# Kernel tuning notes

Measured on AMD Instinct MI355X. Metric: run time of the kernel, lower is better.

The kernel has to match this reference:

```python
import jax, jax.numpy as jnp
import numpy as np

LODS = [16, 32, 64, 128, 256]
SCENE_SCALE = 4.0
DESC = 4
N = 2_000_000
# 8 corner offsets of a voxel, bit-decoded: (x, y, z) in {0,1}^3
_CORNERS = jnp.asarray([[(i >> 2) & 1, (i >> 1) & 1, i & 1] for i in range(8)], dtype=jnp.int32)  # (8,3)


def setup_inputs() -> dict:
    key = jax.random.key(0)
    ks = jax.random.split(key, 2 + len(LODS))
    inp = {
        "pts": jax.random.normal(ks[0], (N, 3), dtype=jnp.float32),
        "d": jax.random.normal(ks[1], (N, 3), dtype=jnp.float32),
    }
    # codebook init mirrors torch: zeros + 0.01 * randn, shape (LOD^3, desc)
    for i, res in enumerate(LODS):
        inp[f"codebook_{i}"] = jax.random.normal(ks[2 + i], (res ** 3, DESC), dtype=jnp.float32) * 0.01
    return inp


def _trilerp(res, codebook, pts01):
    """NGLOD-style dense-grid trilinear interpolation.
    pts01: (N,3) in [0,1]; codebook: (res^3, DESC). Returns (N, DESC)."""
    pos = pts01 * (res - 1)                                   # (N,3) in [0, res-1]
    c0 = jnp.clip(jnp.floor(pos).astype(jnp.int32), 0, res - 2)
    frac = pos - c0.astype(pos.dtype)                         # (N,3) in [0,1]
    idx = c0[:, None, :] + _CORNERS[None, :, :]               # (N,8,3)
    flat = (idx[..., 0] * res + idx[..., 1]) * res + idx[..., 2]  # (N,8) row-major x*res^2+y*res+z
    # trilinear weights: prod over axes of (frac if corner bit set else 1-frac)
    w = jnp.prod(jnp.where(_CORNERS[None] == 1, frac[:, None, :], 1.0 - frac[:, None, :]), axis=-1)  # (N,8)
    return jnp.einsum('nkd,nk->nd', codebook[flat], w)        # gather + weighted sum


def reference(pts, d, codebook_0, codebook_1, codebook_2, codebook_3, codebook_4):
    cbs = (codebook_0, codebook_1, codebook_2, codebook_3, codebook_4)
    p = pts / SCENE_SCALE
    mask = jnp.all(jnp.abs(p) < 0.5, axis=-1)                 # inside unit cube
    p01 = jnp.clip(p + 0.5, 0.0, 1.0)                         # clamp keeps OOB points index-safe; masked out below
    feats = _trilerp(LODS[0], cbs[0], p01)
    for res, cb in zip(LODS[1:], cbs[1:]):
        feats = feats + _trilerp(res, cb, p01)                # sum features across LODs
    color = jnp.where(mask[:, None], feats[:, 0:3], 0.0)      # masked scatter into zero buffer
    log_sigma = jnp.where(mask, feats[:, 3], -100000.0)       # exp(-1e5) underflows to 0, as in torch
    return color, jnp.exp(log_sigma)[:, None]
```

## Files before the change

kernel.cpp:

```cpp
#include <hip/hip_runtime.h>
#include <math.h>

static constexpr float kSceneScale = 4.0f;
static constexpr int   kG     = 16;
static constexpr int   kNBins = kG * kG * kG + 1;
static constexpr int   kNB    = 256;
static constexpr int   kDirectThresh = 48;

static constexpr int kS4 = 18;
static constexpr int kS3 = 10;
static constexpr int kS2 = 6;
static constexpr int kS1 = 4;
static constexpr int kS0 = 3;

__device__ __forceinline__ void fma4(float4& acc, float w, const float4& c) {
    acc.x = fmaf(w, c.x, acc.x);
    acc.y = fmaf(w, c.y, acc.y);
    acc.z = fmaf(w, c.z, acc.z);
    acc.w = fmaf(w, c.w, acc.w);
}

__device__ __forceinline__ unsigned bf16r(float f) {
    unsigned u = __float_as_uint(f);
    return (u + 0x7FFFu + ((u >> 16) & 1u)) >> 16;
}
__device__ __forceinline__ unsigned pk2(float lo, float hi) {
    return bf16r(lo) | (bf16r(hi) << 16);
}
__device__ __forceinline__ float4 bfdec(uint2 w) {
    float4 r;
    r.x = __uint_as_float(w.x << 16);
    r.y = __uint_as_float(w.x & 0xFFFF0000u);
    r.z = __uint_as_float(w.y << 16);
    r.w = __uint_as_float(w.y & 0xFFFF0000u);
    return r;
}

template <int RES>
__device__ __forceinline__ void trilerp_acc(const float4* __restrict__ cb,
                                            float x, float y, float z,
                                            float4& acc) {
    const float s = (float)(RES - 1);
    float fx = x * s, fy = y * s, fz = z * s;
    int x0 = min((int)fx, RES - 2);
    int y0 = min((int)fy, RES - 2);
    int z0 = min((int)fz, RES - 2);
    float tx = fx - (float)x0;
    float ty = fy - (float)y0;
    float tz = fz - (float)z0;
    int base = (x0 * RES + y0) * RES + z0;
    float4 c000 = cb[base];
    float4 c001 = cb[base + 1];
    float4 c010 = cb[base + RES];
    float4 c011 = cb[base + RES + 1];
    float4 c100 = cb[base + RES * RES];
    float4 c101 = cb[base + RES * RES + 1];
    float4 c110 = cb[base + RES * RES + RES];
    float4 c111 = cb[base + RES * RES + RES + 1];
    float wx0 = 1.0f - tx, wx1 = tx;
    float wy0 = 1.0f - ty, wy1 = ty;
    float wz0 = 1.0f - tz, wz1 = tz;
    fma4(acc, wx0 * wy0 * wz0, c000);
    fma4(acc, wx0 * wy0 * wz1, c001);
    fma4(acc, wx0 * wy1 * wz0, c010);
    fma4(acc, wx0 * wy1 * wz1, c011);
    fma4(acc, wx1 * wy0 * wz0, c100);
    fma4(acc, wx1 * wy0 * wz1, c101);
    fma4(acc, wx1 * wy1 * wz0, c110);
    fma4(acc, wx1 * wy1 * wz1, c111);
}

__device__ __forceinline__ void load_p01(const float* __restrict__ pts, int i,
                                         float& x, float& y, float& z, bool& inside) {
    float px = pts[3 * i + 0] * (1.0f / kSceneScale);
    float py = pts[3 * i + 1] * (1.0f / kSceneScale);
    float pz = pts[3 * i + 2] * (1.0f / kSceneScale);
    inside = (fabsf(px) < 0.5f) && (fabsf(py) < 0.5f) && (fabsf(pz) < 0.5f);
    x = fminf(fmaxf(px + 0.5f, 0.0f), 1.0f);
    y = fminf(fmaxf(py + 0.5f, 0.0f), 1.0f);
    z = fminf(fmaxf(pz + 0.5f, 0.0f), 1.0f);
}

__device__ __forceinline__ unsigned point_key(const float* __restrict__ pts, int i) {
    float x, y, z; bool inside;
    load_p01(pts, i, x, y, z, inside);
    if (!inside) return (unsigned)(kNBins - 1);
    int bx = min((int)(x * kG), kG - 1);
    int by = min((int)(y * kG), kG - 1);
    int bz = min((int)(z * kG), kG - 1);
    return (unsigned)((bx * kG + by) * kG + bz);
}

__global__ __launch_bounds__(256) void keys_hist_kernel(
        const float* __restrict__ pts, unsigned* __restrict__ keys,
        unsigned* __restrict__ blockHist, int n, int chunk) {
    __shared__ unsigned hist[kNBins];
    int tid = threadIdx.x;
    for (int j = tid; j < kNBins; j += 256) hist[j] = 0;
    __syncthreads();
    int beg = blockIdx.x * chunk;
    int end = min(n, beg + chunk);
    for (int i = beg + tid; i < end; i += 256) {
        unsigned key = point_key(pts, i);
        keys[i] = key;
        atomicAdd(&hist[key], 1u);
    }
    __syncthreads();
    for (int j = tid; j < kNBins; j += 256) blockHist[(size_t)j * kNB + blockIdx.x] = hist[j];
}

__global__ __launch_bounds__(256) void scan_chunks_kernel(
        unsigned* __restrict__ data, unsigned* __restrict__ partials, int total) {
    __shared__ unsigned sums[256];
    int tid = threadIdx.x;
    int base = blockIdx.x * 1024 + tid * 4;
    uint4 v = make_uint4(0u, 0u, 0u, 0u);
    if (base + 3 < total) {
        v = *(const uint4*)(data + base);
    } else {
        unsigned* p = (unsigned*)&v;
        for (int k = 0; k < 4; ++k) if (base + k < total) p[k] = data[base + k];
    }
    unsigned s1 = v.x + v.y, s2 = s1 + v.z, s3 = s2 + v.w;
    sums[tid] = s3;
    __syncthreads();
    for (int off = 1; off < 256; off <<= 1) {
        unsigned t = (tid >= off) ? sums[tid - off] : 0u;
        __syncthreads();
        sums[tid] += t;
        __syncthreads();
    }
    unsigned excl = sums[tid] - s3;
    uint4 o;
    o.x = excl; o.y = excl + v.x; o.z = excl + s1; o.w = excl + s2;
    if (base + 3 < total) {
        *(uint4*)(data + base) = o;
    } else {
        unsigned* p = (unsigned*)&o;
        for (int k = 0; k < 4; ++k) if (base + k < total) data[base + k] = p[k];
    }
    if (tid == 255) partials[blockIdx.x] = sums[255];
}

__global__ __launch_bounds__(256) void scan_partials_kernel(unsigned* __restrict__ partials, int m) {
    __shared__ unsigned buf[256];
    __shared__ unsigned carry_s;
    int tid = threadIdx.x;
    if (tid == 0) carry_s = 0u;
    __syncthreads();
    for (int base = 0; base < m; base += 256) {
        unsigned v = (base + tid < m) ? partials[base + tid] : 0u;
        buf[tid] = v;
        __syncthreads();
        for (int off = 1; off < 256; off <<= 1) {
            unsigned t = (tid >= off) ? buf[tid - off] : 0u;
            __syncthreads();
            buf[tid] += t;
            __syncthreads();
        }
        unsigned incl = buf[tid];
        unsigned c = carry_s;
        if (base + tid < m) partials[base + tid] = c + incl - v;
        __syncthreads();
        if (tid == 255) carry_s = c + incl;
        __syncthreads();
    }
}

__global__ __launch_bounds__(256) void scan_add_kernel(
        unsigned* __restrict__ data, const unsigned* __restrict__ partials, int total) {
    int tid = threadIdx.x;
    int base = blockIdx.x * 1024 + tid * 4;
    unsigned p = partials[blockIdx.x];
    if (base + 3 < total) {
        uint4 v = *(const uint4*)(data + base);
        v.x += p; v.y += p; v.z += p; v.w += p;
        *(uint4*)(data + base) = v;
    } else {
        for (int k = 0; k < 4; ++k) if (base + k < total) data[base + k] += p;
    }
}

__global__ __launch_bounds__(256) void scatter_kernel(
        const float* __restrict__ pts,
        const unsigned* __restrict__ keys, const unsigned* __restrict__ blockHist,
        float4* __restrict__ spts, float* __restrict__ out, int n, int chunk) {
    __shared__ unsigned offs[kNBins];
    int tid = threadIdx.x;
    for (int j = tid; j < kNBins; j += 256) offs[j] = blockHist[(size_t)j * kNB + blockIdx.x];
    __syncthreads();
    int beg = blockIdx.x * chunk;
    int end = min(n, beg + chunk);
    for (int i = beg + tid; i < end; i += 256) {
        unsigned k = keys[i];
        float x, y, z; bool inside;
        load_p01(pts, i, x, y, z, inside);
        unsigned pos = atomicAdd(&offs[k], 1u);
        if (inside) {
            spts[pos] = make_float4(x, y, z, __uint_as_float((unsigned)i));
        } else {
            out[3 * i + 0] = 0.0f;
            out[3 * i + 1] = 0.0f;
            out[3 * i + 2] = 0.0f;
            out[(size_t)3 * n + i] = 0.0f;
        }
    }
}

template <int RES, int SPAN>
__device__ __forceinline__ void stage_bf16(const float4* __restrict__ cb, uint2* sbuf,
                                           int lox, int loy, int loz, int tid, int nthr) {
    for (int c = tid; c < SPAN * SPAN * SPAN; c += nthr) {
        int cz = c % SPAN;
        int cy = (c / SPAN) % SPAN;
        int cx = c / (SPAN * SPAN);
        int gx = min(lox + cx, RES - 1);
        int gy = min(loy + cy, RES - 1);
        int gz = min(loz + cz, RES - 1);
        float4 v = cb[((size_t)gx * RES + gy) * RES + gz];
        sbuf[c] = make_uint2(pk2(v.x, v.y), pk2(v.z, v.w));
    }
}

template <int RES, int SPAN>
__device__ __forceinline__ void stage_f32(const float4* __restrict__ cb, float4* sbuf,
                                          int lox, int loy, int loz, int tid, int nthr) {
    for (int c = tid; c < SPAN * SPAN * SPAN; c += nthr) {
        int cz = c % SPAN;
        int cy = (c / SPAN) % SPAN;
        int cx = c / (SPAN * SPAN);
        int gx = min(lox + cx, RES - 1);
        int gy = min(loy + cy, RES - 1);
        int gz = min(loz + cz, RES - 1);
        sbuf[c] = cb[((size_t)gx * RES + gy) * RES + gz];
    }
}

template <int RES, int SPAN>
__device__ __forceinline__ void lerp_lds_bf16(const uint2* sbuf,
                                              int lox, int loy, int loz,
                                              float x, float y, float z, float4& acc) {
    const float s = (float)(RES - 1);
    float fx = x * s, fy = y * s, fz = z * s;
    int x0 = min((int)fx, RES - 2);
    int y0 = min((int)fy, RES - 2);
    int z0 = min((int)fz, RES - 2);
    float tx = fx - (float)x0;
    float ty = fy - (float)y0;
    float tz = fz - (float)z0;
    int base = ((x0 - lox) * SPAN + (y0 - loy)) * SPAN + (z0 - loz);
    uint2 w000 = sbuf[base];
    uint2 w001 = sbuf[base + 1];
    uint2 w010 = sbuf[base + SPAN];
    uint2 w011 = sbuf[base + SPAN + 1];
    uint2 w100 = sbuf[base + SPAN * SPAN];
    uint2 w101 = sbuf[base + SPAN * SPAN + 1];
    uint2 w110 = sbuf[base + SPAN * SPAN + SPAN];
    uint2 w111 = sbuf[base + SPAN * SPAN + SPAN + 1];
    float wx0 = 1.0f - tx, wx1 = tx;
    float wy0 = 1.0f - ty, wy1 = ty;
    float wz0 = 1.0f - tz, wz1 = tz;
    fma4(acc, wx0 * wy0 * wz0, bfdec(w000));
    fma4(acc, wx0 * wy0 * wz1, bfdec(w001));
    fma4(acc, wx0 * wy1 * wz0, bfdec(w010));
    fma4(acc, wx0 * wy1 * wz1, bfdec(w011));
    fma4(acc, wx1 * wy0 * wz0, bfdec(w100));
    fma4(acc, wx1 * wy0 * wz1, bfdec(w101));
    fma4(acc, wx1 * wy1 * wz0, bfdec(w110));
    fma4(acc, wx1 * wy1 * wz1, bfdec(w111));
}

template <int RES, int SPAN>
__device__ __forceinline__ void lerp_lds_f32(const float4* sbuf,
                                             int lox, int loy, int loz,
                                             float x, float y, float z, float4& acc) {
    const float s = (float)(RES - 1);
    float fx = x * s, fy = y * s, fz = z * s;
    int x0 = min((int)fx, RES - 2);
    int y0 = min((int)fy, RES - 2);
    int z0 = min((int)fz, RES - 2);
    float tx = fx - (float)x0;
    float ty = fy - (float)y0;
    float tz = fz - (float)z0;
    int base = ((x0 - lox) * SPAN + (y0 - loy)) * SPAN + (z0 - loz);
    float4 c000 = sbuf[base];
    float4 c001 = sbuf[base + 1];
    float4 c010 = sbuf[base + SPAN];
    float4 c011 = sbuf[base + SPAN + 1];
    float4 c100 = sbuf[base + SPAN * SPAN];
    float4 c101 = sbuf[base + SPAN * SPAN + 1];
    float4 c110 = sbuf[base + SPAN * SPAN + SPAN];
    float4 c111 = sbuf[base + SPAN * SPAN + SPAN + 1];
    float wx0 = 1.0f - tx, wx1 = tx;
    float wy0 = 1.0f - ty, wy1 = ty;
    float wz0 = 1.0f - tz, wz1 = tz;
    fma4(acc, wx0 * wy0 * wz0, c000);
    fma4(acc, wx0 * wy0 * wz1, c001);
    fma4(acc, wx0 * wy1 * wz0, c010);
    fma4(acc, wx0 * wy1 * wz1, c011);
    fma4(acc, wx1 * wy0 * wz0, c100);
    fma4(acc, wx1 * wy0 * wz1, c101);
    fma4(acc, wx1 * wy1 * wz0, c110);
    fma4(acc, wx1 * wy1 * wz1, c111);
}

__global__ __launch_bounds__(512) void compute_tiled_kernel(
        const float4* __restrict__ spts,
        const unsigned* __restrict__ blockHist,
        const float4* __restrict__ cb0,
        const float4* __restrict__ cb1,
        const float4* __restrict__ cb2,
        const float4* __restrict__ cb3,
        const float4* __restrict__ cb4,
        float* __restrict__ out,
        int n) {
    int bin = blockIdx.x;
    unsigned start = blockHist[(size_t)bin * kNB];
    unsigned end   = blockHist[(size_t)(bin + 1) * kNB];
    if (start >= end) return;

    int bx = bin >> 8, by = (bin >> 4) & 15, bz = bin & 15;
    int tid = threadIdx.x;

    if ((int)(end - start) < kDirectThresh) {
        for (unsigned t = start + tid; t < end; t += 512) {
            float4 s = spts[t];
            int i = (int)__float_as_uint(s.w);
            float4 acc = make_float4(0.0f, 0.0f, 0.0f, 0.0f);
            trilerp_acc<16>(cb0, s.x, s.y, s.z, acc);
            trilerp_acc<32>(cb1, s.x, s.y, s.z, acc);
            trilerp_acc<64>(cb2, s.x, s.y, s.z, acc);
            trilerp_acc<128>(cb3, s.x, s.y, s.z, acc);
            trilerp_acc<256>(cb4, s.x, s.y, s.z, acc);
            out[3 * i + 0] = acc.x;
            out[3 * i + 1] = acc.y;
            out[3 * i + 2] = acc.z;
            out[(size_t)3 * n + i] = expf(acc.w);
        }
        return;
    }

    __shared__ uint2  s4[kS4 * kS4 * kS4];
    __shared__ uint2  s3[kS3 * kS3 * kS3];
    __shared__ float4 s2[kS2 * kS2 * kS2];
    __shared__ float4 s1[kS1 * kS1 * kS1];
    __shared__ float4 s0[kS0 * kS0 * kS0];

    int lox4 = (bx * 255) >> 4, loy4 = (by * 255) >> 4, loz4 = (bz * 255) >> 4;
    int lox3 = (bx * 127) >> 4, loy3 = (by * 127) >> 4, loz3 = (bz * 127) >> 4;
    int lox2 = (bx * 63) >> 4,  loy2 = (by * 63) >> 4,  loz2 = (bz * 63) >> 4;
    int lox1 = (bx * 31) >> 4,  loy1 = (by * 31) >> 4,  loz1 = (bz * 31) >> 4;
    int lox0 = (bx * 15) >> 4,  loy0 = (by * 15) >> 4,  loz0 = (bz * 15) >> 4;

    stage_bf16<256, kS4>(cb4, s4, lox4, loy4, loz4, tid, 512);
    stage_bf16<128, kS3>(cb3, s3, lox3, loy3, loz3, tid, 512);
    stage_f32<64,  kS2>(cb2, s2, lox2, loy2, loz2, tid, 512);
    stage_f32<32,  kS1>(cb1, s1, lox1, loy1, loz1, tid, 512);
    stage_f32<16,  kS0>(cb0, s0, lox0, loy0, loz0, tid, 512);
    __syncthreads();

    for (unsigned t = start + tid; t < end; t += 512) {
        float4 s = spts[t];
        int i = (int)__float_as_uint(s.w);
        float4 acc = make_float4(0.0f, 0.0f, 0.0f, 0.0f);
        lerp_lds_f32<16,  kS0>(s0, lox0, loy0, loz0, s.x, s.y, s.z, acc);
        lerp_lds_f32<32,  kS1>(s1, lox1, loy1, loz1, s.x, s.y, s.z, acc);
        lerp_lds_f32<64,  kS2>(s2, lox2, loy2, loz2, s.x, s.y, s.z, acc);
        lerp_lds_bf16<128, kS3>(s3, lox3, loy3, loz3, s.x, s.y, s.z, acc);
        lerp_lds_bf16<256, kS4>(s4, lox4, loy4, loz4, s.x, s.y, s.z, acc);
        out[3 * i + 0] = acc.x;
        out[3 * i + 1] = acc.y;
        out[3 * i + 2] = acc.z;
        out[(size_t)3 * n + i] = expf(acc.w);
    }
}

__global__ __launch_bounds__(256) void direct_kernel(
        const float* __restrict__ pts,
        const float4* __restrict__ cb0,
        const float4* __restrict__ cb1,
        const float4* __restrict__ cb2,
        const float4* __restrict__ cb3,
        const float4* __restrict__ cb4,
        float* __restrict__ out,
        int n) {
    int i = blockIdx.x * blockDim.x + threadIdx.x;
    if (i >= n) return;
    float x, y, z; bool inside;
    load_p01(pts, i, x, y, z, inside);
    float c0 = 0.0f, c1 = 0.0f, c2 = 0.0f, sg = 0.0f;
    if (inside) {
        float4 acc = make_float4(0.0f, 0.0f, 0.0f, 0.0f);
        trilerp_acc<16>(cb0, x, y, z, acc);
        trilerp_acc<32>(cb1, x, y, z, acc);
        trilerp_acc<64>(cb2, x, y, z, acc);
        trilerp_acc<128>(cb3, x, y, z, acc);
        trilerp_acc<256>(cb4, x, y, z, acc);
        c0 = acc.x; c1 = acc.y; c2 = acc.z; sg = expf(acc.w);
    }
    out[3 * i + 0] = c0;
    out[3 * i + 1] = c1;
    out[3 * i + 2] = c2;
    out[(size_t)3 * n + i] = sg;
}

extern "C" void kernel_launch(void* const* d_in, const int* in_sizes, int n_in,
                              void* d_out, int out_size, void* d_ws, size_t ws_size,
                              hipStream_t stream) {
    const float* pts = (const float*)d_in[0];
    const float4* cb0 = (const float4*)d_in[2];
    const float4* cb1 = (const float4*)d_in[3];
    const float4* cb2 = (const float4*)d_in[4];
    const float4* cb3 = (const float4*)d_in[5];
    const float4* cb4 = (const float4*)d_in[6];
    float* out = (float*)d_out;

    int n = in_sizes[0] / 3;

    const int histTotal = kNBins * kNB;
    const int nChunks   = (histTotal + 1023) / 1024;

    size_t off_keys = 0;
    size_t off_spts = (off_keys + (size_t)n * 4 + 15) & ~(size_t)15;
    size_t off_hist = off_spts + (size_t)n * 16;
    size_t off_part = off_hist + (size_t)histTotal * 4;
    size_t need     = off_part + (size_t)nChunks * 4;

    dim3 block(256);
    int nwg = (n + 255) / 256;

    if (ws_size < need) {
        direct_kernel<<<dim3(nwg), block, 0, stream>>>(pts, cb0, cb1, cb2, cb3, cb4, out, n);
        return;
    }

    unsigned* keys      = (unsigned*)((char*)d_ws + off_keys);
    float4*   spts      = (float4*)((char*)d_ws + off_spts);
    unsigned* blockHist = (unsigned*)((char*)d_ws + off_hist);
    unsigned* partials  = (unsigned*)((char*)d_ws + off_part);

    int chunk = (n + kNB - 1) / kNB;

    keys_hist_kernel<<<dim3(kNB), block, 0, stream>>>(pts, keys, blockHist, n, chunk);
    scan_chunks_kernel<<<dim3(nChunks), block, 0, stream>>>(blockHist, partials, histTotal);
    scan_partials_kernel<<<dim3(1), block, 0, stream>>>(partials, nChunks);
    scan_add_kernel<<<dim3(nChunks), block, 0, stream>>>(blockHist, partials, histTotal);
    scatter_kernel<<<dim3(kNB), block, 0, stream>>>(pts, keys, blockHist, spts, out, n, chunk);
    compute_tiled_kernel<<<dim3(kG * kG * kG), dim3(512), 0, stream>>>(
        spts, blockHist, cb0, cb1, cb2, cb3, cb4, out, n);
}
```

Measured before the change: 320.7 us.

## Align bins to finest-LOD cells and stage only the 256-res codebook in LDS

Point binning now uses the finest-level cell index (x*255 shifted by 4), so each bin maps exactly onto a 16-cell tile of the 256^3 grid and the LDS halo shrinks from 18 to 17. Only the finest codebook is staged into LDS as bf16. The four coarser levels are read directly from global memory, since they are small and likely cache-resident. Launch bounds now ask for 8 waves per SIMD. The intent is to cut LDS footprint and staging work per block so more blocks fit per CU, at the cost of extra global/cache gathers for the coarse levels.

```diff
diff --git a/kernel.cpp b/kernel.cpp
--- a/kernel.cpp
+++ b/kernel.cpp
@@ -6,12 +6,7 @@
 static constexpr int   kNBins = kG * kG * kG + 1;
 static constexpr int   kNB    = 256;
 static constexpr int   kDirectThresh = 48;
-
-static constexpr int kS4 = 18;
-static constexpr int kS3 = 10;
-static constexpr int kS2 = 6;
-static constexpr int kS1 = 4;
-static constexpr int kS0 = 3;
+static constexpr int   kS4 = 17;
 
 __device__ __forceinline__ void fma4(float4& acc, float w, const float4& c) {
     acc.x = fmaf(w, c.x, acc.x);
@@ -85,10 +80,10 @@
     float x, y, z; bool inside;
     load_p01(pts, i, x, y, z, inside);
     if (!inside) return (unsigned)(kNBins - 1);
-    int bx = min((int)(x * kG), kG - 1);
-    int by = min((int)(y * kG), kG - 1);
-    int bz = min((int)(z * kG), kG - 1);
-    return (unsigned)((bx * kG + by) * kG + bz);
+    int x0 = min((int)(x * 255.0f), 254) >> 4;
+    int y0 = min((int)(y * 255.0f), 254) >> 4;
+    int z0 = min((int)(z * 255.0f), 254) >> 4;
+    return (unsigned)((x0 * kG + y0) * kG + z0);
 }
 
 __global__ __launch_bounds__(256) void keys_hist_kernel(
@@ -207,104 +202,7 @@
     }
 }
 
-template <int RES, int SPAN>
-__device__ __forceinline__ void stage_bf16(const float4* __restrict__ cb, uint2* sbuf,
-                                           int lox, int loy, int loz, int tid, int nthr) {
-    for (int c = tid; c < SPAN * SPAN * SPAN; c += nthr) {
-        int cz = c % SPAN;
-        int cy = (c / SPAN) % SPAN;
-        int cx = c / (SPAN * SPAN);
-        int gx = min(lox + cx, RES - 1);
-        int gy = min(loy + cy, RES - 1);
-        int gz = min(loz + cz, RES - 1);
-        float4 v = cb[((size_t)gx * RES + gy) * RES + gz];
-        sbuf[c] = make_uint2(pk2(v.x, v.y), pk2(v.z, v.w));
-    }
-}
-
-template <int RES, int SPAN>
-__device__ __forceinline__ void stage_f32(const float4* __restrict__ cb, float4* sbuf,
-                                          int lox, int loy, int loz, int tid, int nthr) {
-    for (int c = tid; c < SPAN * SPAN * SPAN; c += nthr) {
-        int cz = c % SPAN;
-        int cy = (c / SPAN) % SPAN;
-        int cx = c / (SPAN * SPAN);
-        int gx = min(lox + cx, RES - 1);
-        int gy = min(loy + cy, RES - 1);
-        int gz = min(loz + cz, RES - 1);
-        sbuf[c] = cb[((size_t)gx * RES + gy) * RES + gz];
-    }
-}
-
-template <int RES, int SPAN>
-__device__ __forceinline__ void lerp_lds_bf16(const uint2* sbuf,
-                                              int lox, int loy, int loz,
-                                              float x, float y, float z, float4& acc) {
-    const float s = (float)(RES - 1);
-    float fx = x * s, fy = y * s, fz = z * s;
-    int x0 = min((int)fx, RES - 2);
-    int y0 = min((int)fy, RES - 2);
-    int z0 = min((int)fz, RES - 2);
-    float tx = fx - (float)x0;
-    float ty = fy - (float)y0;
-    float tz = fz - (float)z0;
-    int base = ((x0 - lox) * SPAN + (y0 - loy)) * SPAN + (z0 - loz);
-    uint2 w000 = sbuf[base];
-    uint2 w001 = sbuf[base + 1];
-    uint2 w010 = sbuf[base + SPAN];
-    uint2 w011 = sbuf[base + SPAN + 1];
-    uint2 w100 = sbuf[base + SPAN * SPAN];
-    uint2 w101 = sbuf[base + SPAN * SPAN + 1];
-    uint2 w110 = sbuf[base + SPAN * SPAN + SPAN];
-    uint2 w111 = sbuf[base + SPAN * SPAN + SPAN + 1];
-    float wx0 = 1.0f - tx, wx1 = tx;
-    float wy0 = 1.0f - ty, wy1 = ty;
-    float wz0 = 1.0f - tz, wz1 = tz;
-    fma4(acc, wx0 * wy0 * wz0, bfdec(w000));
-    fma4(acc, wx0 * wy0 * wz1, bfdec(w001));
-    fma4(acc, wx0 * wy1 * wz0, bfdec(w010));
-    fma4(acc, wx0 * wy1 * wz1, bfdec(w011));
-    fma4(acc, wx1 * wy0 * wz0, bfdec(w100));
-    fma4(acc, wx1 * wy0 * wz1, bfdec(w101));
-    fma4(acc, wx1 * wy1 * wz0, bfdec(w110));
-    fma4(acc, wx1 * wy1 * wz1, bfdec(w111));
-}
-
-template <int RES, int SPAN>
-__device__ __forceinline__ void lerp_lds_f32(const float4* sbuf,
-                                             int lox, int loy, int loz,
-                                             float x, float y, float z, float4& acc) {
-    const float s = (float)(RES - 1);
-    float fx = x * s, fy = y * s, fz = z * s;
-    int x0 = min((int)fx, RES - 2);
-    int y0 = min((int)fy, RES - 2);
-    int z0 = min((int)fz, RES - 2);
-    float tx = fx - (float)x0;
-    float ty = fy - (float)y0;
-    float tz = fz - (float)z0;
-    int base = ((x0 - lox) * SPAN + (y0 - loy)) * SPAN + (z0 - loz);
-    float4 c000 = sbuf[base];
-    float4 c001 = sbuf[base + 1];
-    float4 c010 = sbuf[base + SPAN];
-    float4 c011 = sbuf[base + SPAN + 1];
-    float4 c100 = sbuf[base + SPAN * SPAN];
-    float4 c101 = sbuf[base + SPAN * SPAN + 1];
-    float4 c110 = sbuf[base + SPAN * SPAN + SPAN];
-    float4 c111 = sbuf[base + SPAN * SPAN + SPAN + 1];
-    float wx0 = 1.0f - tx, wx1 = tx;
-    float wy0 = 1.0f - ty, wy1 = ty;
-    float wz0 = 1.0f - tz, wz1 = tz;
-    fma4(acc, wx0 * wy0 * wz0, c000);
-    fma4(acc, wx0 * wy0 * wz1, c001);
-    fma4(acc, wx0 * wy1 * wz0, c010);
-    fma4(acc, wx0 * wy1 * wz1, c011);
-    fma4(acc, wx1 * wy0 * wz0, c100);
-    fma4(acc, wx1 * wy0 * wz1, c101);
-    fma4(acc, wx1 * wy1 * wz0, c110);
-    fma4(acc, wx1 * wy1 * wz1, c111);
-}
-
-__global__ __launch_bounds__(512) void compute_tiled_kernel(
+__global__ __launch_bounds__(512, 8) void compute_tiled_kernel(
         const float4* __restrict__ spts,
         const unsigned* __restrict__ blockHist,
         const float4* __restrict__ cb0,
@@ -319,7 +217,6 @@
     unsigned end   = blockHist[(size_t)(bin + 1) * kNB];
     if (start >= end) return;
 
-    int bx = bin >> 8, by = (bin >> 4) & 15, bz = bin & 15;
     int tid = threadIdx.x;
 
     if ((int)(end - start) < kDirectThresh) {
@@ -340,34 +237,62 @@
         return;
     }
 
-    __shared__ uint2  s4[kS4 * kS4 * kS4];
-    __shared__ uint2  s3[kS3 * kS3 * kS3];
-    __shared__ float4 s2[kS2 * kS2 * kS2];
-    __shared__ float4 s1[kS1 * kS1 * kS1];
-    __shared__ float4 s0[kS0 * kS0 * kS0];
-
-    int lox4 = (bx * 255) >> 4, loy4 = (by * 255) >> 4, loz4 = (bz * 255) >> 4;
-    int lox3 = (bx * 127) >> 4, loy3 = (by * 127) >> 4, loz3 = (bz * 127) >> 4;
-    int lox2 = (bx * 63) >> 4,  loy2 = (by * 63) >> 4,  loz2 = (bz * 63) >> 4;
-    int lox1 = (bx * 31) >> 4,  loy1 = (by * 31) >> 4,  loz1 = (bz * 31) >> 4;
-    int lox0 = (bx * 15) >> 4,  loy0 = (by * 15) >> 4,  loz0 = (bz * 15) >> 4;
-
-    stage_bf16<256, kS4>(cb4, s4, lox4, loy4, loz4, tid, 512);
-    stage_bf16<128, kS3>(cb3, s3, lox3, loy3, loz3, tid, 512);
-    stage_f32<64,  kS2>(cb2, s2, lox2, loy2, loz2, tid, 512);
-    stage_f32<32,  kS1>(cb1, s1, lox1, loy1, loz1, tid, 512);
-    stage_f32<16,  kS0>(cb0, s0, lox0, loy0, loz0, tid, 512);
+    __shared__ uint2 s4[kS4 * kS4 * kS4];
+
+    int bx = bin >> 8, by = (bin >> 4) & 15, bz = bin & 15;
+    int ox = bx << 4, oy = by << 4, oz = bz << 4;
+
+    for (int c = tid; c < kS4 * kS4 * kS4; c += 512) {
+        int cz = c % kS4;
+        int cy = (c / kS4) % kS4;
+        int cx = c / (kS4 * kS4);
+        int gx = min(ox + cx, 255);
+        int gy = min(oy + cy, 255);
+        int gz = min(oz + cz, 255);
+        float4 v = cb4[((size_t)gx * 256 + gy) * 256 + gz];
+        s4[c] = make_uint2(pk2(v.x, v.y), pk2(v.z, v.w));
+    }
     __syncthreads();
 
     for (unsigned t = start + tid; t < end; t += 512) {
         float4 s = spts[t];
         int i = (int)__float_as_uint(s.w);
         float4 acc = make_float4(0.0f, 0.0f, 0.0f, 0.0f);
-        lerp_lds_f32<16,  kS0>(s0, lox0, loy0, loz0, s.x, s.y, s.z, acc);
-        lerp_lds_f32<32,  kS1>(s1, lox1, loy1, loz1, s.x, s.y, s.z, acc);
-        lerp_lds_f32<64,  kS2>(s2, lox2, loy2, loz2, s.x, s.y, s.z, acc);
-        lerp_lds_bf16<128, kS3>(s3, lox3, loy3, loz3, s.x, s.y, s.z, acc);
-        lerp_lds_bf16<256, kS4>(s4, lox4, loy4, loz4, s.x, s.y, s.z, acc);
+        trilerp_acc<16>(cb0, s.x, s.y, s.z, acc);
+        trilerp_acc<32>(cb1, s.x, s.y, s.z, acc);
+        trilerp_acc<64>(cb2, s.x, s.y, s.z, acc);
+        trilerp_acc<128>(cb3, s.x, s.y, s.z, acc);
+
+        {
+            float fx = s.x * 255.0f, fy = s.y * 255.0f, fz = s.z * 255.0f;
+            int x0 = min((int)fx, 254);
+            int y0 = min((int)fy, 254);
+            int z0 = min((int)fz, 254);
+            float tx = fx - (float)x0;
+            float ty = fy - (float)y0;
+            float tz = fz - (float)z0;
+            int base = ((x0 - ox) * kS4 + (y0 - oy)) * kS4 + (z0 - oz);
+            uint2 w000 = s4[base];
+            uint2 w001 = s4[base + 1];
+            uint2 w010 = s4[base + kS4];
+            uint2 w011 = s4[base + kS4 + 1];
+            uint2 w100 = s4[base + kS4 * kS4];
+            uint2 w101 = s4[base + kS4 * kS4 + 1];
+            uint2 w110 = s4[base + kS4 * kS4 + kS4];
+            uint2 w111 = s4[base + kS4 * kS4 + kS4 + 1];
+            float wx0 = 1.0f - tx, wx1 = tx;
+            float wy0 = 1.0f - ty, wy1 = ty;
+            float wz0 = 1.0f - tz, wz1 = tz;
+            fma4(acc, wx0 * wy0 * wz0, bfdec(w000));
+            fma4(acc, wx0 * wy0 * wz1, bfdec(w001));
+            fma4(acc, wx0 * wy1 * wz0, bfdec(w010));
+            fma4(acc, wx0 * wy1 * wz1, bfdec(w011));
+            fma4(acc, wx1 * wy0 * wz0, bfdec(w100));
+            fma4(acc, wx1 * wy0 * wz1, bfdec(w101));
+            fma4(acc, wx1 * wy1 * wz0, bfdec(w110));
+            fma4(acc, wx1 * wy1 * wz1, bfdec(w111));
+        }
+
         out[3 * i + 0] = acc.x;
         out[3 * i + 1] = acc.y;
         out[3 * i + 2] = acc.z;
```

Result: no change. 317.8 us (-0.9%).
